# Kernel optimization log

Hardware: AMD Instinct MI355X
Metric: run time of the kernel (lower is better)

The kernel has to match this reference:

```python
import jax, jax.numpy as jnp
import numpy as np

B, S, D, H = 4, 2048, 1024, 16
HD = D // H          # head_dim = 64; per-head scale = sqrt(HD) as in source
FF = 4096
EPS = 1e-5


def _layernorm(x, g, b):
    m = jnp.mean(x, axis=-1, keepdims=True)
    v = jnp.mean(jnp.square(x - m), axis=-1, keepdims=True)
    return (x - m) * jax.lax.rsqrt(v + EPS) * g + b


def setup_inputs() -> dict:
    key = jax.random.key(0)
    ks = jax.random.split(key, 10)
    std = 0.02
    return {
        "x": jax.random.normal(ks[0], (B, S, D), jnp.float32),
        "wq": jax.random.normal(ks[1], (H, D, HD), jnp.float32) * std,
        "bq": jnp.zeros((H, HD), jnp.float32),
        "wk": jax.random.normal(ks[2], (H, D, HD), jnp.float32) * std,
        "bk": jnp.zeros((H, HD), jnp.float32),
        "wv": jax.random.normal(ks[3], (H, D, HD), jnp.float32) * std,
        "bv": jnp.zeros((H, HD), jnp.float32),
        "wo": jax.random.normal(ks[4], (D, D), jnp.float32) * std,
        "bo": jnp.zeros((D,), jnp.float32),
        "w1": jax.random.normal(ks[5], (D, FF), jnp.float32) * std,
        "b1": jnp.zeros((FF,), jnp.float32),
        "w2": jax.random.normal(ks[6], (FF, D), jnp.float32) * std,
        "b2": jnp.zeros((D,), jnp.float32),
        "g1": jnp.ones((D,), jnp.float32),
        "beta1": jnp.zeros((D,), jnp.float32),
        "g2": jnp.ones((D,), jnp.float32),
        "beta2": jnp.zeros((D,), jnp.float32),
    }


def reference(x, wq, bq, wk, bk, wv, bv, wo, bo, w1, b1, w2, b2, g1, beta1, g2, beta2):
    # Per-head Q/K/V projections (stacked over heads) -> [B,H,S,HD]
    q = jnp.einsum('bsd,hdf->bhsf', x, wq) + bq[None, :, None, :]
    k = jnp.einsum('bsd,hdf->bhsf', x, wk) + bk[None, :, None, :]
    v = jnp.einsum('bsd,hdf->bhsf', x, wv) + bv[None, :, None, :]

    scale = jnp.sqrt(jnp.asarray(HD, jnp.float32))
    att = jnp.einsum('bhqf,bhkf->bhqk', q, k) / scale  # [B,H,S,S]
    causal = jnp.tril(jnp.ones((S, S), dtype=bool))
    att = jnp.where(causal[None, None], att, -jnp.inf)
    p = jax.nn.softmax(att, axis=-1)
    o = jnp.einsum('bhqk,bhkf->bhqf', p, v)            # [B,H,S,HD]
    o = o.transpose(0, 2, 1, 3).reshape(B, S, D)       # concat heads
    attn_out = o @ wo + bo

    h = _layernorm(x + attn_out, g1, beta1)            # post-LN, dropout=0 (eval)
    ff = jax.nn.gelu(h @ w1 + b1, approximate=False) @ w2 + b2
    return _layernorm(h + ff, g2, beta2)
```

## Files before the change

kernel.cpp:

```cpp
#include <hip/hip_runtime.h>
#include <hip/hip_bf16.h>
#include <math.h>

typedef __bf16 bf16x8 __attribute__((ext_vector_type(8)));
typedef float floatx4 __attribute__((ext_vector_type(4)));
typedef unsigned short ushort8 __attribute__((ext_vector_type(8)));
typedef unsigned short ushort4v __attribute__((ext_vector_type(4)));

__device__ __forceinline__ unsigned short f2bs(float f){
  union { float f; unsigned u; } v; v.f = f;
  unsigned r = v.u + 0x7fffu + ((v.u >> 16) & 1u);
  return (unsigned short)(r >> 16);
}
__device__ __forceinline__ float bs2f(unsigned short s){
  union { unsigned u; float f; } v; v.u = ((unsigned)s) << 16; return v.f;
}
__device__ __forceinline__ unsigned pk2(float a, float b){
  union { __hip_bfloat162 h; unsigned u; } cv;
  cv.h = __float22bfloat162_rn(make_float2(a, b));
  return cv.u;
}
__device__ __forceinline__ void gl_lds16(const void* g, void* l){
  __builtin_amdgcn_global_load_lds(
      (const __attribute__((address_space(1))) void*)g,
      (__attribute__((address_space(3))) void*)l,
      16, 0, 0);
}

__global__ __launch_bounds__(256) void cvt_x(const float* __restrict__ x,
                                             unsigned short* __restrict__ o){
  const int i = (blockIdx.x*256 + threadIdx.x)*4;
  const float4 v = *(const float4*)(x + i);
  ushort4v u = { f2bs(v.x), f2bs(v.y), f2bs(v.z), f2bs(v.w) };
  *(ushort4v*)(o + i) = u;
}

__global__ __launch_bounds__(256) void transpose_pack(const float* __restrict__ src,
                                                      unsigned short* __restrict__ dst,
                                                      int R, int C){
  __shared__ float tile[32][65];
  const int r0 = blockIdx.y*32, c0 = blockIdx.x*64;
  const int t = threadIdx.x;
  {
    const int r = t >> 3, cc = (t & 7)*8;
    const float* p = src + (size_t)(r0+r)*C + c0 + cc;
    const float4 v0 = *(const float4*)p;
    const float4 v1 = *(const float4*)(p+4);
    tile[r][cc+0]=v0.x; tile[r][cc+1]=v0.y; tile[r][cc+2]=v0.z; tile[r][cc+3]=v0.w;
    tile[r][cc+4]=v1.x; tile[r][cc+5]=v1.y; tile[r][cc+6]=v1.z; tile[r][cc+7]=v1.w;
  }
  __syncthreads();
  const int f = t >> 2, rr = (t & 3)*8;
  ushort8 u;
  #pragma unroll
  for (int j=0;j<8;j++) u[j] = f2bs(tile[rr+j][f]);
  *(ushort8*)(dst + (size_t)(c0+f)*R + r0 + rr) = u;
}

__global__ __launch_bounds__(256) void pack_qkv(const float* __restrict__ wq,
                                                const float* __restrict__ wk,
                                                const float* __restrict__ wv,
                                                const float* __restrict__ bq,
                                                const float* __restrict__ bk,
                                                const float* __restrict__ bv,
                                                unsigned short* __restrict__ Wt,
                                                float* __restrict__ Bc){
  __shared__ float tile[32][65];
  const int dt = blockIdx.x, h = blockIdx.y, sel = blockIdx.z;
  const float* src = (sel==0 ? wq : (sel==1 ? wk : wv)) + (size_t)h*65536;
  const int t = threadIdx.x, d0 = dt*32;
  {
    const int r = t >> 3, cc = (t & 7)*8;
    const float* p = src + (size_t)(d0+r)*64 + cc;
    const float4 v0 = *(const float4*)p;
    const float4 v1 = *(const float4*)(p+4);
    tile[r][cc+0]=v0.x; tile[r][cc+1]=v0.y; tile[r][cc+2]=v0.z; tile[r][cc+3]=v0.w;
    tile[r][cc+4]=v1.x; tile[r][cc+5]=v1.y; tile[r][cc+6]=v1.z; tile[r][cc+7]=v1.w;
  }
  __syncthreads();
  const int f = t >> 2, rr = (t & 3)*8;
  ushort8 u;
  #pragma unroll
  for (int j=0;j<8;j++) u[j] = f2bs(tile[rr+j][f]);
  const size_t n = (size_t)sel*1024 + h*64 + f;
  *(ushort8*)(Wt + n*1024 + d0 + rr) = u;
  if (dt==0 && t<64){
    const float* bs = (sel==0 ? bq : (sel==1 ? bk : bv)) + h*64;
    Bc[sel*1024 + h*64 + t] = bs[t];
  }
}

template<int MODE>
__global__ __launch_bounds__(256, 4)
void gemm_tn(const unsigned short* __restrict__ A,
             const unsigned short* __restrict__ Bt,
             const float* __restrict__ bias,
             void* __restrict__ out0,
             void* __restrict__ out1,
             void* __restrict__ out2,
             int K, int OW, int klen){
  __shared__ __align__(16) unsigned short As[128*32];
  __shared__ __align__(16) unsigned short Bs[128*32];
  const int tid = threadIdx.x;
  const int wave = tid >> 6, lane = tid & 63;
  const int quad = lane >> 4, l15 = lane & 15;
  const int lin = blockIdx.x;
  const int n0 = (lin & 63) << 7;
  const int m0 = (lin >> 6) << 7;
  const int kz = blockIdx.z;
  const int kbase = kz * klen;
  const int wr = (wave >> 1) << 6, wc = (wave & 1) << 6;

  floatx4 acc[4][4];
  #pragma unroll
  for (int i=0;i<4;i++)
    #pragma unroll
    for (int j=0;j<4;j++) acc[i][j] = (floatx4)0.0f;

  const unsigned short* gA[2];
  const unsigned short* gB[2];
  int lofs[2];
  #pragma unroll
  for (int r2=0;r2<2;r2++){
    const int slot = r2*256 + tid;
    const int rp = slot >> 3, rem = slot & 7;
    const int row = rp*2 + (rem >> 2);
    const int kc = (rem & 3) ^ (rp & 3);
    gA[r2] = A  + (size_t)(m0 + row)*K + kbase + kc*8;
    gB[r2] = Bt + (size_t)(n0 + row)*K + kbase + kc*8;
    lofs[r2] = slot*8;
  }
  int aofs[4], bofs[4];
  #pragma unroll
  for (int t=0;t<4;t++){
    const int ra = wr + t*16 + l15;
    aofs[t] = (ra>>1)*64 + (ra&1)*32 + ((quad ^ ((ra>>1)&3))<<3);
    const int rb = wc + t*16 + l15;
    bofs[t] = (rb>>1)*64 + (rb&1)*32 + ((quad ^ ((rb>>1)&3))<<3);
  }

  for (int k0 = 0; k0 < klen; k0 += 32){
    gl_lds16(gA[0] + k0, As + lofs[0]);
    gl_lds16(gA[1] + k0, As + lofs[1]);
    gl_lds16(gB[0] + k0, Bs + lofs[0]);
    gl_lds16(gB[1] + k0, Bs + lofs[1]);
    __syncthreads();
    bf16x8 af[4];
    #pragma unroll
    for (int t=0;t<4;t++) af[t] = *(const bf16x8*)(&As[aofs[t]]);
    #pragma unroll
    for (int j=0;j<4;j++){
      const bf16x8 bv = *(const bf16x8*)(&Bs[bofs[j]]);
      #pragma unroll
      for (int i=0;i<4;i++)
        acc[i][j] = __builtin_amdgcn_mfma_f32_16x16x32_bf16(af[i], bv, acc[i][j], 0,0,0);
    }
    __syncthreads();
  }

  #pragma unroll
  for (int i=0;i<4;i++){
    const int row0 = m0 + wr + i*16 + quad*4;
    float4 b4 = make_float4(0.f,0.f,0.f,0.f);
    if (MODE != 4 || kz == 0) b4 = *(const float4*)(bias + row0);
    #pragma unroll
    for (int j=0;j<4;j++){
      const int tok = n0 + wc + j*16 + l15;
      float v0 = acc[i][j][0] + b4.x;
      float v1 = acc[i][j][1] + b4.y;
      float v2 = acc[i][j][2] + b4.z;
      float v3 = acc[i][j][3] + b4.w;
      if (MODE == 1){
        float4 o4; o4.x=v0; o4.y=v1; o4.z=v2; o4.w=v3;
        *(float4*)((float*)out0 + (size_t)tok*OW + row0) = o4;
      } else if (MODE == 2){
        float vv[4] = {v0,v1,v2,v3};
        #pragma unroll
        for (int r=0;r<4;r++){
          const float v = vv[r];
          const float u = 0.7978845608f*v*(1.0f + 0.044715f*v*v);
          const float e = __builtin_amdgcn_exp2f(u * 2.885390082f);
          vv[r] = 0.5f*v*(1.0f + (1.0f - 2.0f/(1.0f + e)));
        }
        uint2 pkd = make_uint2(pk2(vv[0], vv[1]), pk2(vv[2], vv[3]));
        *(uint2*)((unsigned short*)out0 + (size_t)tok*4096 + row0) = pkd;
      } else if (MODE == 4){
        uint2 pkd = make_uint2(pk2(v0, v1), pk2(v2, v3));
        unsigned short* o = (unsigned short*)(kz ? out1 : out0);
        *(uint2*)(o + (size_t)tok*1024 + row0) = pkd;
      } else {
        if (row0 < 1024){
          const float s = 0.18033688011112042f;
          uint2 pkd = make_uint2(pk2(v0*s, v1*s), pk2(v2*s, v3*s));
          *(uint2*)((unsigned short*)out0 + (size_t)tok*1024 + row0) = pkd;
        } else if (row0 < 2048){
          uint2 pkd = make_uint2(pk2(v0, v1), pk2(v2, v3));
          *(uint2*)((unsigned short*)out1 + (size_t)tok*1024 + (row0-1024)) = pkd;
        } else {
          uint2 pkd = make_uint2(pk2(v0, v1), pk2(v2, v3));
          *(uint2*)((unsigned short*)out2 + (size_t)tok*1024 + (row0-2048)) = pkd;
        }
      }
    }
  }
}

#define NOOP ((void)0)
#define VMCNT4 asm volatile("s_waitcnt vmcnt(4)" ::: "memory")
#define VMCNT0 asm volatile("s_waitcnt vmcnt(0)" ::: "memory")
#define TAILW { if (tg < NT-2) VMCNT4; else VMCNT0; }

#define STAGE_A(T, H) { const int T_ = (T); if (T_ < NT){                     \
    unsigned short* l_ = lds + (T_&1)*32768 + (H)*8192;                       \
    const int ko_ = kbase + (T_<<6);                                          \
    gl_lds16(srcA##H##_0 + ko_, l_ + ch0*8);                                  \
    gl_lds16(srcA##H##_1 + ko_, l_ + ch1*8); } }
#define STAGE_B(T, H) { const int T_ = (T); if (T_ < NT){                     \
    unsigned short* l_ = lds + (T_&1)*32768 + 16384 + (H)*8192;               \
    const int ko_ = kbase + (T_<<6);                                          \
    gl_lds16(srcB##H##_0 + ko_, l_ + ch0*8);                                  \
    gl_lds16(srcB##H##_1 + ko_, l_ + ch1*8); } }

#define PHASE_SYNC                                                            \
    __builtin_amdgcn_s_barrier();                                             \
    asm volatile("s_waitcnt lgkmcnt(0)" ::: "memory");                        \
    __builtin_amdgcn_sched_barrier(0);                                        \
    __builtin_amdgcn_s_setprio(1);

#define MFMA_Q(AF, BF, MH, NH)                                                \
    _Pragma("unroll")                                                         \
    for (int k_=0;k_<2;k_++)                                                  \
      _Pragma("unroll")                                                       \
      for (int m_=0;m_<4;m_++)                                                \
        _Pragma("unroll")                                                     \
        for (int n_=0;n_<2;n_++)                                              \
          acc[(MH)*4+m_][(NH)*2+n_] = __builtin_amdgcn_mfma_f32_16x16x32_bf16( \
              AF[m_][k_], BF[n_][k_], acc[(MH)*4+m_][(NH)*2+n_], 0,0,0);

template<int MODE>
__global__ __launch_bounds__(512, 2)
void gemm256(const unsigned short* __restrict__ A,
             const unsigned short* __restrict__ Bt,
             const float* __restrict__ bias,
             void* __restrict__ out0,
             void* __restrict__ out1,
             void* __restrict__ out2,
             int K, int klen){
  __shared__ __align__(16) unsigned short lds[65536];
  const int tid = threadIdx.x;
  const int wave = tid >> 6, lane = tid & 63;
  const int quad = lane >> 4, l15 = lane & 15;
  const int wm = wave >> 2, wn = wave & 3;
  const int lin = blockIdx.x;
  const int n0 = (lin & 31) << 8;
  const int m0 = (lin >> 5) << 8;
  const int kz = blockIdx.z;
  const int kbase = kz * klen;
  const int NT = klen >> 6;

  const int r0 = tid >> 3;
  const int r1 = r0 + 64;
  const int g0 = (tid & 7) ^ (r0 & 7);
  const int ch0 = tid, ch1 = tid + 512;

  const unsigned short* srcA0_0 = A  + (size_t)(m0 +       r0)*K + g0*8;
  const unsigned short* srcA0_1 = A  + (size_t)(m0 +       r1)*K + g0*8;
  const unsigned short* srcA1_0 = A  + (size_t)(m0 + 128 + r0)*K + g0*8;
  const unsigned short* srcA1_1 = A  + (size_t)(m0 + 128 + r1)*K + g0*8;
  const unsigned short* srcB0_0 = Bt + (size_t)(n0 +       r0)*K + g0*8;
  const unsigned short* srcB0_1 = Bt + (size_t)(n0 +       r1)*K + g0*8;
  const unsigned short* srcB1_0 = Bt + (size_t)(n0 + 128 + r0)*K + g0*8;
  const unsigned short* srcB1_1 = Bt + (size_t)(n0 + 128 + r1)*K + g0*8;

  const int xr = l15 & 7;
  int aoff[4][2], boff[2][2];
  #pragma unroll
  for (int m=0;m<4;m++){
    const int rh = wm*64 + m*16 + l15;
    #pragma unroll
    for (int k=0;k<2;k++)
      aoff[m][k] = rh*64 + (((k*4 + quad) ^ xr) << 3);
  }
  #pragma unroll
  for (int n=0;n<2;n++){
    const int rb = wn*32 + n*16 + l15;
    #pragma unroll
    for (int k=0;k<2;k++)
      boff[n][k] = rb*64 + (((k*4 + quad) ^ xr) << 3);
  }

  floatx4 acc[8][4];
  #pragma unroll
  for (int i=0;i<8;i++)
    #pragma unroll
    for (int j=0;j<4;j++) acc[i][j] = (floatx4)0.0f;

  STAGE_B(0,0); STAGE_A(0,0); STAGE_A(0,1); STAGE_B(0,1);
  STAGE_B(1,0); STAGE_A(1,0);
  VMCNT4;
  __builtin_amdgcn_s_barrier();

  for (int tg = 0; tg < NT; ++tg){
    const int d = tg & 1;
    const unsigned short* A0b = lds + d*32768;
    const unsigned short* A1b = A0b + 8192;
    const unsigned short* B0b = lds + d*32768 + 16384;
    const unsigned short* B1b = B0b + 8192;
    bf16x8 af0[4][2], af1[4][2], bf0[2][2], bf1[2][2];

    #pragma unroll
    for (int m_=0;m_<4;m_++)
      #pragma unroll
      for (int k_=0;k_<2;k_++) af0[m_][k_] = *(const bf16x8*)(A0b + aoff[m_][k_]);
    #pragma unroll
    for (int n_=0;n_<2;n_++)
      #pragma unroll
      for (int k_=0;k_<2;k_++) bf0[n_][k_] = *(const bf16x8*)(B0b + boff[n_][k_]);
    STAGE_A(tg+1, 1);
    PHASE_SYNC;
    MFMA_Q(af0, bf0, 0, 0);
    __builtin_amdgcn_s_setprio(0);
    __builtin_amdgcn_s_barrier();

    #pragma unroll
    for (int n_=0;n_<2;n_++)
      #pragma unroll
      for (int k_=0;k_<2;k_++) bf1[n_][k_] = *(const bf16x8*)(B1b + boff[n_][k_]);
    STAGE_B(tg+1, 1);
    PHASE_SYNC;
    MFMA_Q(af0, bf1, 0, 1);
    __builtin_amdgcn_s_setprio(0);
    __builtin_amdgcn_s_barrier();

    #pragma unroll
    for (int m_=0;m_<4;m_++)
      #pragma unroll
      for (int k_=0;k_<2;k_++) af1[m_][k_] = *(const bf16x8*)(A1b + aoff[m_][k_]);
    STAGE_B(tg+2, 0);
    PHASE_SYNC;
    MFMA_Q(af1, bf1, 1, 1);
    __builtin_amdgcn_s_setprio(0);
    __builtin_amdgcn_s_barrier();

    STAGE_A(tg+2, 0);
    PHASE_SYNC;
    MFMA_Q(af1, bf0, 1, 0);
    __builtin_amdgcn_s_setprio(0);
    TAILW;
    __builtin_amdgcn_s_barrier();
  }

  #pragma unroll
  for (int mh=0; mh<2; mh++){
    #pragma unroll
    for (int m=0; m<4; m++){
      const int row0 = m0 + mh*128 + wm*64 + m*16 + quad*4;
      float4 b4 = make_float4(0.f,0.f,0.f,0.f);
      if (MODE != 4 || kz == 0) b4 = *(const float4*)(bias + row0);
      #pragma unroll
      for (int nh=0; nh<2; nh++){
        #pragma unroll
        for (int n=0; n<2; n++){
          const int tok = n0 + nh*128 + wn*32 + n*16 + l15;
          const floatx4 a = acc[mh*4+m][nh*2+n];
          float v0 = a[0]+b4.x, v1 = a[1]+b4.y, v2 = a[2]+b4.z, v3 = a[3]+b4.w;
          if (MODE == 2){
            float vv[4] = {v0,v1,v2,v3};
            #pragma unroll
            for (int r=0;r<4;r++){
              const float v = vv[r];
              const float u = 0.7978845608f*v*(1.0f + 0.044715f*v*v);
              const float e = __builtin_amdgcn_exp2f(u * 2.885390082f);
              vv[r] = 0.5f*v*(1.0f + (1.0f - 2.0f/(1.0f + e)));
            }
            uint2 pkd = make_uint2(pk2(vv[0], vv[1]), pk2(vv[2], vv[3]));
            *(uint2*)((unsigned short*)out0 + (size_t)tok*4096 + row0) = pkd;
          } else if (MODE == 4){
            uint2 pkd = make_uint2(pk2(v0, v1), pk2(v2, v3));
            unsigned short* o = (unsigned short*)(kz ? out1 : out0);
            *(uint2*)(o + (size_t)tok*1024 + row0) = pkd;
          } else {
            if (row0 < 1024){
              const float s = 0.18033688011112042f;
              uint2 pkd = make_uint2(pk2(v0*s, v1*s), pk2(v2*s, v3*s));
              *(uint2*)((unsigned short*)out0 + (size_t)tok*1024 + row0) = pkd;
            } else if (row0 < 2048){
              uint2 pkd = make_uint2(pk2(v0, v1), pk2(v2, v3));
              *(uint2*)((unsigned short*)out1 + (size_t)tok*1024 + (row0-1024)) = pkd;
            } else {
              uint2 pkd = make_uint2(pk2(v0, v1), pk2(v2, v3));
              *(uint2*)((unsigned short*)out2 + (size_t)tok*1024 + (row0-2048)) = pkd;
            }
          }
        }
      }
    }
  }
}

__global__ __launch_bounds__(256) void vtrans(const unsigned short* __restrict__ Vtok,
                                              unsigned short* __restrict__ Vt){
  __shared__ unsigned short tile[64][65];
  const int st = blockIdx.x, bh = blockIdx.y;
  const int b = bh >> 4, h = bh & 15;
  const int t = threadIdx.x;
  {
    const int r = t >> 2, cc = (t & 3) * 16;
    const unsigned short* src = Vtok + (size_t)((b<<11) + (st<<6) + r)*1024 + (h<<6) + cc;
    ushort8 u0 = *(const ushort8*)src;
    ushort8 u1 = *(const ushort8*)(src + 8);
    #pragma unroll
    for (int j=0;j<8;j++){ tile[r][cc+j] = u0[j]; tile[r][cc+8+j] = u1[j]; }
  }
  __syncthreads();
  const int f = t >> 2, ss = (t & 3) * 16;
  ushort8 w0, w1;
  #pragma unroll
  for (int j=0;j<8;j++){ w0[j] = tile[ss+j][f]; w1[j] = tile[ss+8+j][f]; }
  unsigned short* dst = Vt + (size_t)bh*64*2048 + (size_t)f*2048 + (st<<6) + ss;
  *(ushort8*)dst = w0;
  *(ushort8*)(dst + 8) = w1;
}

__global__ __launch_bounds__(256, 4) void attn(const unsigned short* __restrict__ Q,
                                               const unsigned short* __restrict__ Kg,
                                               const unsigned short* __restrict__ Vt,
                                               unsigned short* __restrict__ O){
  __shared__ __align__(16) unsigned short Ks[64*64];
  __shared__ __align__(16) unsigned short Vs[64*64];
  __shared__ __align__(16) unsigned short PT[4][2][16*68];

  const int lin = blockIdx.x;
  const int bh = lin & 63;
  const int qt_lo = lin >> 6;
  const int qt_hi = 31 - qt_lo;
  const int b = bh >> 4, h = bh & 15;
  const int tid = threadIdx.x, wave = tid >> 6, lane = tid & 63;
  const int quad = lane >> 4, l15 = lane & 15;
  const float FM = 12.0f;

  const size_t qbase = (size_t)((b<<11) + (wave<<4) + l15)*1024 + (h<<6);
  bf16x8 qf_hi[2], qf_lo[2];
  qf_hi[0] = *(const bf16x8*)(Q + qbase + (size_t)(qt_hi<<6)*1024 + quad*8);
  qf_hi[1] = *(const bf16x8*)(Q + qbase + (size_t)(qt_hi<<6)*1024 + 32 + quad*8);
  qf_lo[0] = *(const bf16x8*)(Q + qbase + (size_t)(qt_lo<<6)*1024 + quad*8);
  qf_lo[1] = *(const bf16x8*)(Q + qbase + (size_t)(qt_lo<<6)*1024 + 32 + quad*8);

  floatx4 oa_hi[4], oa_lo[4];
  #pragma unroll
  for (int i=0;i<4;i++){ oa_hi[i] = (floatx4)0.0f; oa_lo[i] = (floatx4)0.0f; }
  float li_hi = 0.0f, li_lo = 0.0f;

  const unsigned short* Kbh = Kg + ((size_t)(b<<11))*1024 + (h<<6);
  const unsigned short* Vbh = Vt + (size_t)bh*64*2048;
  unsigned short* Pw0 = &PT[wave][0][0];
  unsigned short* Pw1 = &PT[wave][1][0];

  const int slot0 = wave*128 + lane;
  const int krow0 = slot0 >> 3, kc0 = (slot0 & 7) ^ (krow0 & 7);
  const int slot1 = slot0 + 64;
  const int krow1 = slot1 >> 3, kc1 = (slot1 & 7) ^ (krow1 & 7);

  auto softmax_P = [&](floatx4* sa, float& li, unsigned short* Pbuf, bool diag){
    if (diag){
      const int qrow = (wave<<4) + l15;
      #pragma unroll
      for (int tj=0;tj<4;tj++)
        #pragma unroll
        for (int r=0;r<4;r++)
          if (tj*16 + quad*4 + r > qrow) sa[tj][r] = -1e30f;
    }
    float rs = 0.0f;
    #pragma unroll
    for (int tj=0;tj<4;tj++)
      #pragma unroll
      for (int r=0;r<4;r++){
        const float p = __builtin_amdgcn_exp2f(sa[tj][r] - FM);
        sa[tj][r] = p;
        rs += p;
      }
    li += rs;
    #pragma unroll
    for (int tj=0;tj<4;tj++){
      uint2 pkd = make_uint2(pk2(sa[tj][0], sa[tj][1]), pk2(sa[tj][2], sa[tj][3]));
      *(uint2*)(Pbuf + l15*68 + tj*16 + quad*4) = pkd;
    }
  };

  for (int kt = 0; kt <= qt_hi; ++kt){
    gl_lds16(Kbh + (size_t)((kt<<6) + krow0)*1024 + kc0*8, Ks + wave*1024);
    gl_lds16(Kbh + (size_t)((kt<<6) + krow1)*1024 + kc1*8, Ks + wave*1024 + 512);
    gl_lds16(Vbh + (size_t)krow0*2048 + (kt<<6) + kc0*8, Vs + wave*1024);
    gl_lds16(Vbh + (size_t)krow1*2048 + (kt<<6) + kc1*8, Vs + wave*1024 + 512);
    __syncthreads();

    if (kt <= qt_lo){
      floatx4 sh[4], sl[4];
      __builtin_amdgcn_s_setprio(1);
      #pragma unroll
      for (int tj=0;tj<4;tj++){
        sh[tj] = (floatx4)0.0f; sl[tj] = (floatx4)0.0f;
        #pragma unroll
        for (int ks=0;ks<2;ks++){
          const int n = tj*16 + l15;
          const int c = (ks*4 + quad) ^ (n & 7);
          const bf16x8 kf = *(const bf16x8*)(Ks + n*64 + c*8);
          sh[tj] = __builtin_amdgcn_mfma_f32_16x16x32_bf16(kf, qf_hi[ks], sh[tj], 0,0,0);
          sl[tj] = __builtin_amdgcn_mfma_f32_16x16x32_bf16(kf, qf_lo[ks], sl[tj], 0,0,0);
        }
      }
      __builtin_amdgcn_s_setprio(0);
      softmax_P(sh, li_hi, Pw0, false);
      softmax_P(sl, li_lo, Pw1, kt == qt_lo);
      __builtin_amdgcn_s_setprio(1);
      #pragma unroll
      for (int ks2=0;ks2<2;ks2++){
        const bf16x8 pfh = *(const bf16x8*)(Pw0 + l15*68 + ks2*32 + quad*8);
        const bf16x8 pfl = *(const bf16x8*)(Pw1 + l15*68 + ks2*32 + quad*8);
        #pragma unroll
        for (int tn=0;tn<4;tn++){
          const int n2 = tn*16 + l15;
          const int c = (ks2*4 + quad) ^ (n2 & 7);
          const bf16x8 vf = *(const bf16x8*)(Vs + n2*64 + c*8);
          oa_hi[tn] = __builtin_amdgcn_mfma_f32_16x16x32_bf16(vf, pfh, oa_hi[tn], 0,0,0);
          oa_lo[tn] = __builtin_amdgcn_mfma_f32_16x16x32_bf16(vf, pfl, oa_lo[tn], 0,0,0);
        }
      }
      __builtin_amdgcn_s_setprio(0);
    } else {
      floatx4 sh[4];
      __builtin_amdgcn_s_setprio(1);
      #pragma unroll
      for (int tj=0;tj<4;tj++){
        sh[tj] = (floatx4)0.0f;
        #pragma unroll
        for (int ks=0;ks<2;ks++){
          const int n = tj*16 + l15;
          const int c = (ks*4 + quad) ^ (n & 7);
          const bf16x8 kf = *(const bf16x8*)(Ks + n*64 + c*8);
          sh[tj] = __builtin_amdgcn_mfma_f32_16x16x32_bf16(kf, qf_hi[ks], sh[tj], 0,0,0);
        }
      }
      __builtin_amdgcn_s_setprio(0);
      softmax_P(sh, li_hi, Pw0, kt == qt_hi);
      __builtin_amdgcn_s_setprio(1);
      #pragma unroll
      for (int ks2=0;ks2<2;ks2++){
        const bf16x8 pfh = *(const bf16x8*)(Pw0 + l15*68 + ks2*32 + quad*8);
        #pragma unroll
        for (int tn=0;tn<4;tn++){
          const int n2 = tn*16 + l15;
          const int c = (ks2*4 + quad) ^ (n2 & 7);
          const bf16x8 vf = *(const bf16x8*)(Vs + n2*64 + c*8);
          oa_hi[tn] = __builtin_amdgcn_mfma_f32_16x16x32_bf16(vf, pfh, oa_hi[tn], 0,0,0);
        }
      }
      __builtin_amdgcn_s_setprio(0);
    }
    __syncthreads();
  }

  li_hi += __shfl_xor(li_hi, 16, 64);
  li_hi += __shfl_xor(li_hi, 32, 64);
  li_lo += __shfl_xor(li_lo, 16, 64);
  li_lo += __shfl_xor(li_lo, 32, 64);
  {
    const float inv = 1.0f / li_hi;
    unsigned short* Orow = O + (size_t)((b<<11) + (qt_hi<<6) + (wave<<4) + l15)*1024 + (h<<6);
    #pragma unroll
    for (int tn=0;tn<4;tn++){
      uint2 pkd = make_uint2(pk2(oa_hi[tn][0]*inv, oa_hi[tn][1]*inv),
                             pk2(oa_hi[tn][2]*inv, oa_hi[tn][3]*inv));
      *(uint2*)(Orow + tn*16 + quad*4) = pkd;
    }
  }
  {
    const float inv = 1.0f / li_lo;
    unsigned short* Orow = O + (size_t)((b<<11) + (qt_lo<<6) + (wave<<4) + l15)*1024 + (h<<6);
    #pragma unroll
    for (int tn=0;tn<4;tn++){
      uint2 pkd = make_uint2(pk2(oa_lo[tn][0]*inv, oa_lo[tn][1]*inv),
                             pk2(oa_lo[tn][2]*inv, oa_lo[tn][3]*inv));
      *(uint2*)(Orow + tn*16 + quad*4) = pkd;
    }
  }
}

__global__ __launch_bounds__(256) void ln_res(const float* __restrict__ a,
                                              const float* __restrict__ bsrc,
                                              const float* __restrict__ g,
                                              const float* __restrict__ be,
                                              float* __restrict__ of,
                                              unsigned short* __restrict__ ob){
  __shared__ float red1[4], red2[4];
  const int row = blockIdx.x, t = threadIdx.x;
  const int wave = t >> 6, lane = t & 63;
  const float4 va = *(const float4*)(a + (size_t)row*1024 + t*4);
  const float4 vb = *(const float4*)(bsrc + (size_t)row*1024 + t*4);
  float xs[4] = {va.x+vb.x, va.y+vb.y, va.z+vb.z, va.w+vb.w};
  float s = xs[0]+xs[1]+xs[2]+xs[3];
  #pragma unroll
  for (int d=1; d<64; d<<=1) s += __shfl_xor(s, d, 64);
  if (lane==0) red1[wave] = s;
  __syncthreads();
  const float mean = (red1[0]+red1[1]+red1[2]+red1[3]) * (1.0f/1024.0f);
  float vsum = 0.0f;
  #pragma unroll
  for (int i=0;i<4;i++){ const float d = xs[i]-mean; vsum += d*d; }
  #pragma unroll
  for (int d=1; d<64; d<<=1) vsum += __shfl_xor(vsum, d, 64);
  if (lane==0) red2[wave] = vsum;
  __syncthreads();
  const float var = (red2[0]+red2[1]+red2[2]+red2[3]) * (1.0f/1024.0f);
  const float rs = rsqrtf(var + 1e-5f);
  const float4 gg = *(const float4*)(g + t*4);
  const float4 bb = *(const float4*)(be + t*4);
  float y[4];
  y[0] = (xs[0]-mean)*rs*gg.x + bb.x;
  y[1] = (xs[1]-mean)*rs*gg.y + bb.y;
  y[2] = (xs[2]-mean)*rs*gg.z + bb.z;
  y[3] = (xs[3]-mean)*rs*gg.w + bb.w;
  if (of){
    float4 o4; o4.x=y[0]; o4.y=y[1]; o4.z=y[2]; o4.w=y[3];
    *(float4*)(of + (size_t)row*1024 + t*4) = o4;
  }
  if (ob){
    ushort4v u = { f2bs(y[0]), f2bs(y[1]), f2bs(y[2]), f2bs(y[3]) };
    *(ushort4v*)(ob + (size_t)row*1024 + t*4) = u;
  }
}

__global__ __launch_bounds__(256) void ln_res2(const float* __restrict__ a,
                                               const unsigned short* __restrict__ p0,
                                               const unsigned short* __restrict__ p1,
                                               const float* __restrict__ g,
                                               const float* __restrict__ be,
                                               float* __restrict__ of){
  __shared__ float red1[4], red2[4];
  const int row = blockIdx.x, t = threadIdx.x;
  const int wave = t >> 6, lane = t & 63;
  const float4 va = *(const float4*)(a + (size_t)row*1024 + t*4);
  const ushort4v u0 = *(const ushort4v*)(p0 + (size_t)row*1024 + t*4);
  const ushort4v u1 = *(const ushort4v*)(p1 + (size_t)row*1024 + t*4);
  float xs[4] = { va.x + bs2f(u0[0]) + bs2f(u1[0]),
                  va.y + bs2f(u0[1]) + bs2f(u1[1]),
                  va.z + bs2f(u0[2]) + bs2f(u1[2]),
                  va.w + bs2f(u0[3]) + bs2f(u1[3]) };
  float s = xs[0]+xs[1]+xs[2]+xs[3];
  #pragma unroll
  for (int d=1; d<64; d<<=1) s += __shfl_xor(s, d, 64);
  if (lane==0) red1[wave] = s;
  __syncthreads();
  const float mean = (red1[0]+red1[1]+red1[2]+red1[3]) * (1.0f/1024.0f);
  float vsum = 0.0f;
  #pragma unroll
  for (int i=0;i<4;i++){ const float d = xs[i]-mean; vsum += d*d; }
  #pragma unroll
  for (int d=1; d<64; d<<=1) vsum += __shfl_xor(vsum, d, 64);
  if (lane==0) red2[wave] = vsum;
  __syncthreads();
  const float var = (red2[0]+red2[1]+red2[2]+red2[3]) * (1.0f/1024.0f);
  const float rs = rsqrtf(var + 1e-5f);
  const float4 gg = *(const float4*)(g + t*4);
  const float4 bb = *(const float4*)(be + t*4);
  float4 o4;
  o4.x = (xs[0]-mean)*rs*gg.x + bb.x;
  o4.y = (xs[1]-mean)*rs*gg.y + bb.y;
  o4.z = (xs[2]-mean)*rs*gg.z + bb.z;
  o4.w = (xs[3]-mean)*rs*gg.w + bb.w;
  *(float4*)(of + (size_t)row*1024 + t*4) = o4;
}

extern "C" void kernel_launch(void* const* d_in, const int* in_sizes, int n_in,
                              void* d_out, int out_size, void* d_ws, size_t ws_size,
                              hipStream_t stream){
  (void)in_sizes; (void)n_in; (void)out_size; (void)ws_size;
  const float* x  = (const float*)d_in[0];
  const float* wq = (const float*)d_in[1];
  const float* bq = (const float*)d_in[2];
  const float* wk = (const float*)d_in[3];
  const float* bk = (const float*)d_in[4];
  const float* wv = (const float*)d_in[5];
  const float* bv = (const float*)d_in[6];
  const float* wo = (const float*)d_in[7];
  const float* bo = (const float*)d_in[8];
  const float* w1 = (const float*)d_in[9];
  const float* b1 = (const float*)d_in[10];
  const float* w2 = (const float*)d_in[11];
  const float* b2 = (const float*)d_in[12];
  const float* g1 = (const float*)d_in[13];
  const float* be1= (const float*)d_in[14];
  const float* g2 = (const float*)d_in[15];
  const float* be2= (const float*)d_in[16];
  float* out = (float*)d_out;

  char* ws = (char*)d_ws;
  size_t off = 0;
  auto take = [&](size_t bytes)->char*{
    char* p = ws + off; off += (bytes + 255) & ~(size_t)255; return p;
  };
  unsigned short* Xb  = (unsigned short*)take(8192UL*1024*2);
  unsigned short* Qb  = (unsigned short*)take(8192UL*1024*2);
  unsigned short* Kb  = (unsigned short*)take(8192UL*1024*2);
  unsigned short* Vtb = (unsigned short*)take(8192UL*1024*2);
  unsigned short* Ob  = (unsigned short*)take(8192UL*1024*2);
  unsigned short* Midb= Qb;
  unsigned short* Vtok= (unsigned short*)take(8192UL*1024*2);
  unsigned short* Wqkv= (unsigned short*)take(3072UL*1024*2);
  float*          Bqkv= (float*)take(3072UL*4);
  unsigned short* Wot = (unsigned short*)take(1024UL*1024*2);
  unsigned short* W1t = (unsigned short*)take(4096UL*1024*2);
  unsigned short* W2t = (unsigned short*)take(1024UL*4096*2);
  float*          C1  = (float*)take(8192UL*1024*4);
  unsigned short* F0  = (unsigned short*)C1;
  unsigned short* F1  = F0 + 8192UL*1024;
  float*          Hf  = (float*)take(8192UL*1024*4);
  unsigned short* Hb  = (unsigned short*)take(8192UL*1024*2);

  cvt_x<<<8192, 256, 0, stream>>>(x, Xb);
  pack_qkv<<<dim3(32,16,3), 256, 0, stream>>>(wq, wk, wv, bq, bk, bv, Wqkv, Bqkv);
  transpose_pack<<<dim3(16,32),  256, 0, stream>>>(wo, Wot, 1024, 1024);
  transpose_pack<<<dim3(64,32),  256, 0, stream>>>(w1, W1t, 1024, 4096);
  transpose_pack<<<dim3(16,128), 256, 0, stream>>>(w2, W2t, 4096, 1024);

  gemm256<3><<<12*32, 512, 0, stream>>>(Wqkv, Xb, Bqkv, Qb, Kb, Vtok, 1024, 1024);
  vtrans<<<dim3(32,64), 256, 0, stream>>>(Vtok, Vtb);

  attn<<<1024, 256, 0, stream>>>(Qb, Kb, Vtb, Ob);

  gemm_tn<1><<<8*64, 256, 0, stream>>>(Wot, Ob, bo, C1, nullptr, nullptr, 1024, 1024, 1024);
  ln_res<<<8192, 256, 0, stream>>>(x, C1, g1, be1, Hf, Hb);

  gemm256<2><<<16*32, 512, 0, stream>>>(W1t, Hb, b1, Midb, nullptr, nullptr, 1024, 1024);
  gemm256<4><<<dim3(4*32,1,2), 512, 0, stream>>>(W2t, Midb, b2, F0, F1, nullptr, 4096, 2048);
  ln_res2<<<8192, 256, 0, stream>>>(Hf, F0, F1, g2, be2, out);
}
```

Measured before the change: 521.2 us.

## Software-pipeline LDS fragment reads with MFMA phases and drop per-phase barriers

Restructures the GEMM main loop so the LDS fragment reads for the next phase are issued before the current MFMA block. Partial lgkmcnt waits let reads overlap with matrix math, and the A0/B0 fragments for the next k-tile are prefetched across the loop boundary. Workgroup barriers per tile drop from four to two, cutting synchronisation stalls. In exchange it needs more live fragment registers and relies on the hand-counted lgkmcnt values and reduced barriers to keep LDS reuse correct.

```diff
diff --git a/kernel.cpp b/kernel.cpp
--- a/kernel.cpp
+++ b/kernel.cpp
@@ -205,10 +205,12 @@
   }
 }
 
-#define NOOP ((void)0)
 #define VMCNT4 asm volatile("s_waitcnt vmcnt(4)" ::: "memory")
 #define VMCNT0 asm volatile("s_waitcnt vmcnt(0)" ::: "memory")
 #define TAILW { if (tg < NT-2) VMCNT4; else VMCNT0; }
+#define LGKM4 { asm volatile("s_waitcnt lgkmcnt(4)" ::: "memory"); __builtin_amdgcn_sched_barrier(0); }
+#define LGKM8 { asm volatile("s_waitcnt lgkmcnt(8)" ::: "memory"); __builtin_amdgcn_sched_barrier(0); }
+#define LGKM0 { asm volatile("s_waitcnt lgkmcnt(0)" ::: "memory"); __builtin_amdgcn_sched_barrier(0); }
 
 #define STAGE_A(T, H) { const int T_ = (T); if (T_ < NT){                     \
     unsigned short* l_ = lds + (T_&1)*32768 + (H)*8192;                       \
@@ -221,13 +223,8 @@
     gl_lds16(srcB##H##_0 + ko_, l_ + ch0*8);                                  \
     gl_lds16(srcB##H##_1 + ko_, l_ + ch1*8); } }
 
-#define PHASE_SYNC                                                            \
-    __builtin_amdgcn_s_barrier();                                             \
-    asm volatile("s_waitcnt lgkmcnt(0)" ::: "memory");                        \
-    __builtin_amdgcn_sched_barrier(0);                                        \
-    __builtin_amdgcn_s_setprio(1);
-
 #define MFMA_Q(AF, BF, MH, NH)                                                \
+    __builtin_amdgcn_s_setprio(1);                                            \
     _Pragma("unroll")                                                         \
     for (int k_=0;k_<2;k_++)                                                  \
       _Pragma("unroll")                                                       \
@@ -235,7 +232,19 @@
         _Pragma("unroll")                                                     \
         for (int n_=0;n_<2;n_++)                                              \
           acc[(MH)*4+m_][(NH)*2+n_] = __builtin_amdgcn_mfma_f32_16x16x32_bf16( \
-              AF[m_][k_], BF[n_][k_], acc[(MH)*4+m_][(NH)*2+n_], 0,0,0);
+              AF[m_][k_], BF[n_][k_], acc[(MH)*4+m_][(NH)*2+n_], 0,0,0);      \
+    __builtin_amdgcn_s_setprio(0);
+
+#define RD_A(DST, BASE)                                                       \
+    _Pragma("unroll")                                                         \
+    for (int m_=0;m_<4;m_++)                                                  \
+      _Pragma("unroll")                                                       \
+      for (int k_=0;k_<2;k_++) DST[m_][k_] = *(const bf16x8*)((BASE) + aoff[m_][k_]);
+#define RD_B(DST, BASE)                                                       \
+    _Pragma("unroll")                                                         \
+    for (int n_=0;n_<2;n_++)                                                  \
+      _Pragma("unroll")                                                       \
+      for (int k_=0;k_<2;k_++) DST[n_][k_] = *(const bf16x8*)((BASE) + boff[n_][k_]);
 
 template<int MODE>
 __global__ __launch_bounds__(512, 2)
@@ -295,59 +304,45 @@
     #pragma unroll
     for (int j=0;j<4;j++) acc[i][j] = (floatx4)0.0f;
 
+  bf16x8 af0[4][2], af1[4][2], bf0[2][2], bf1[2][2];
+
   STAGE_B(0,0); STAGE_A(0,0); STAGE_A(0,1); STAGE_B(0,1);
   STAGE_B(1,0); STAGE_A(1,0);
   VMCNT4;
   __builtin_amdgcn_s_barrier();
+  RD_A(af0, lds);
+  RD_B(bf0, lds + 16384);
 
   for (int tg = 0; tg < NT; ++tg){
     const int d = tg & 1;
-    const unsigned short* A0b = lds + d*32768;
-    const unsigned short* A1b = A0b + 8192;
-    const unsigned short* B0b = lds + d*32768 + 16384;
-    const unsigned short* B1b = B0b + 8192;
-    bf16x8 af0[4][2], af1[4][2], bf0[2][2], bf1[2][2];
-
-    #pragma unroll
-    for (int m_=0;m_<4;m_++)
-      #pragma unroll
-      for (int k_=0;k_<2;k_++) af0[m_][k_] = *(const bf16x8*)(A0b + aoff[m_][k_]);
-    #pragma unroll
-    for (int n_=0;n_<2;n_++)
-      #pragma unroll
-      for (int k_=0;k_<2;k_++) bf0[n_][k_] = *(const bf16x8*)(B0b + boff[n_][k_]);
+    const unsigned short* A1b = lds + d*32768 + 8192;
+    const unsigned short* B1b = lds + d*32768 + 16384 + 8192;
+
+    RD_B(bf1, B1b);
     STAGE_A(tg+1, 1);
-    PHASE_SYNC;
+    LGKM4;
     MFMA_Q(af0, bf0, 0, 0);
-    __builtin_amdgcn_s_setprio(0);
+
+    RD_A(af1, A1b);
+    STAGE_B(tg+1, 1);
+    LGKM8;
+    MFMA_Q(af0, bf1, 0, 1);
     __builtin_amdgcn_s_barrier();
 
-    #pragma unroll
-    for (int n_=0;n_<2;n_++)
-      #pragma unroll
-      for (int k_=0;k_<2;k_++) bf1[n_][k_] = *(const bf16x8*)(B1b + boff[n_][k_]);
-    STAGE_B(tg+1, 1);
-    PHASE_SYNC;
-    MFMA_Q(af0, bf1, 0, 1);
-    __builtin_amdgcn_s_setprio(0);
-    __builtin_amdgcn_s_barrier();
-
-    #pragma unroll
-    for (int m_=0;m_<4;m_++)
-      #pragma unroll
-      for (int k_=0;k_<2;k_++) af1[m_][k_] = *(const bf16x8*)(A1b + aoff[m_][k_]);
     STAGE_B(tg+2, 0);
-    PHASE_SYNC;
+    LGKM0;
     MFMA_Q(af1, bf1, 1, 1);
-    __builtin_amdgcn_s_setprio(0);
-    __builtin_amdgcn_s_barrier();
 
     STAGE_A(tg+2, 0);
-    PHASE_SYNC;
-    MFMA_Q(af1, bf0, 1, 0);
-    __builtin_amdgcn_s_setprio(0);
     TAILW;
     __builtin_amdgcn_s_barrier();
+    {
+      const unsigned short* A0n = lds + (d^1)*32768;
+      const unsigned short* B0n = A0n + 16384;
+      if (tg+1 < NT){ RD_A(af0, A0n); }
+      MFMA_Q(af1, bf0, 1, 0);
+      if (tg+1 < NT){ RD_B(bf0, B0n); }
+    }
   }
 
   #pragma unroll
```

Result: faster. 500.2 us (-4.0%).
